# Kernel tuning notes

Measured on AMD Instinct MI355X. Metric: run time of the kernel, lower is better.

## Reference

```python
import jax, jax.numpy as jnp
import numpy as np

QLEN, BSZ, DM, NH, DH, FF = 1024, 4, 512, 8, 64, 2048
EPS = 1e-5


def layer_norm(x, g, b):
    mu = x.mean(-1, keepdims=True)
    var = ((x - mu) ** 2).mean(-1, keepdims=True)
    return (x - mu) / jnp.sqrt(var + EPS) * g + b


def rel_pos_emb(qlen, klen, d_model, bsz):
    # XLNet-style 'bi' relative positional encoding: positions klen .. -qlen+1
    freq = jnp.arange(0, d_model, 2, dtype=jnp.float32)
    inv_freq = 1.0 / (10000.0 ** (freq / d_model))
    pos_seq = jnp.arange(klen, -qlen, -1, dtype=jnp.float32)  # [klen+qlen]
    sinusoid = pos_seq[:, None] * inv_freq[None, :]           # [klen+qlen, d/2]
    pe = jnp.concatenate([jnp.sin(sinusoid), jnp.cos(sinusoid)], -1)
    return jnp.broadcast_to(pe[:, None, :], (pe.shape[0], bsz, d_model))


def rel_shift(x, klen):
    # x: [q, p, b, n] with p = klen + qlen
    q, p, b, n = x.shape
    x = x.reshape(p, q, b, n)[1:]
    x = x.reshape(q, p - 1, b, n)[:, :klen]
    return x


def setup_inputs() -> dict:
    key = jax.random.key(0)
    ks = jax.random.split(key, 20)
    s = 0.02
    inp = {
        'src': jax.random.normal(ks[0], (QLEN, BSZ, DM), jnp.float32),
        'q_w': jax.random.normal(ks[1], (DM, NH, DH), jnp.float32) * s,
        'k_w': jax.random.normal(ks[2], (DM, NH, DH), jnp.float32) * s,
        'v_w': jax.random.normal(ks[3], (DM, NH, DH), jnp.float32) * s,
        'r_w': jax.random.normal(ks[4], (DM, NH, DH), jnp.float32) * s,
        'o_w': jax.random.normal(ks[5], (DM, NH, DH), jnp.float32) * s,
        'r_w_bias': jax.random.normal(ks[6], (NH, DH), jnp.float32) * s,
        'r_r_bias': jax.random.normal(ks[7], (NH, DH), jnp.float32) * s,
        'w1': jax.random.normal(ks[8], (FF, DM), jnp.float32) * s,
        'b1': jnp.zeros((FF,), jnp.float32),
        'w2': jax.random.normal(ks[9], (DM, FF), jnp.float32) * s,
        'b2': jnp.zeros((DM,), jnp.float32),
        'g1': jnp.ones((DM,), jnp.float32), 'be1': jnp.zeros((DM,), jnp.float32),
        'g2': jnp.ones((DM,), jnp.float32), 'be2': jnp.zeros((DM,), jnp.float32),
        'gf': jnp.ones((DM,), jnp.float32), 'bf': jnp.zeros((DM,), jnp.float32),
        'src_mask': jnp.triu(jnp.ones((QLEN, QLEN), bool), k=1),
    }
    return inp


def reference(src, q_w, k_w, v_w, r_w, o_w, r_w_bias, r_r_bias,
              w1, b1, w2, b2, g1, be1, g2, be2, gf, bf, src_mask):
    qlen, bsz, dm = src.shape
    klen = qlen  # mems=None
    scale = 1.0 / (DH ** 0.5)
    pos_emb = rel_pos_emb(qlen, klen, dm, bsz)  # [klen+qlen, b, d]
    mask = src_mask.astype(src.dtype)

    # --- RelativeMultiheadAttention (single weight-shared encoder layer) ---
    cat = src  # no memory
    q_head = jnp.einsum('ibh,hnd->ibnd', src, q_w)
    k_head = jnp.einsum('ibh,hnd->ibnd', cat, k_w)
    v_head = jnp.einsum('ibh,hnd->ibnd', cat, v_w)
    k_pos = jnp.einsum('ibh,hnd->ibnd', pos_emb, r_w)

    ac = jnp.einsum('ibnd,jbnd->ijbn', q_head + r_w_bias, k_head)
    bd = jnp.einsum('ibnd,jbnd->ijbn', q_head + r_r_bias, k_pos)
    bd = rel_shift(bd, klen)

    score = (ac + bd) * scale - 1e30 * mask[:, :, None, None]
    prob = jax.nn.softmax(score, axis=1)
    attn_vec = jnp.einsum('ijbn,jbnd->ibnd', prob, v_head)
    attn_out = jnp.einsum('ibnd,hnd->ibh', attn_vec, o_w)

    x = layer_norm(src + attn_out, g1, be1)
    ffn = jax.nn.gelu(x @ w1.T + b1, approximate=False) @ w2.T + b2
    x = layer_norm(x + ffn, g2, be2)

    # final encoder norm
    out = layer_norm(x, gf, bf)
    return out
```

## Files before the change

### kernel.cpp

```cpp
#include <hip/hip_runtime.h>

#define QLEN 1024
#define BSZ  4
#define DM   512
#define NH   8
#define DH   64
#define FFD  2048

static constexpr float LN_EPS = 1e-5f;

typedef __attribute__((ext_vector_type(8))) short short8_t;
typedef __attribute__((ext_vector_type(4))) float f32x4;

__device__ __forceinline__ ushort f2b(float f) {
  uint u = __float_as_uint(f);
  return (ushort)((u + 0x7FFFu + ((u >> 16) & 1u)) >> 16);
}
__device__ __forceinline__ float b2f(ushort h) {
  return __uint_as_float(((uint)h) << 16);
}

__device__ __forceinline__ void cvt8_body(const float* in, ushort* out, int idx) {
  const float4 f0 = *reinterpret_cast<const float4*>(in + (size_t)idx * 8);
  const float4 f1 = *reinterpret_cast<const float4*>(in + (size_t)idx * 8 + 4);
  uint p0 = f2b(f0.x) | ((uint)f2b(f0.y) << 16);
  uint p1 = f2b(f0.z) | ((uint)f2b(f0.w) << 16);
  uint p2 = f2b(f1.x) | ((uint)f2b(f1.y) << 16);
  uint p3 = f2b(f1.z) | ((uint)f2b(f1.w) << 16);
  int4 st; st.x = (int)p0; st.y = (int)p1; st.z = (int)p2; st.w = (int)p3;
  *reinterpret_cast<int4*>(out + (size_t)idx * 8) = st;
}

__global__ __launch_bounds__(256) void prep_kernel(
    const float* __restrict__ src, const float* __restrict__ o_w,
    const float* __restrict__ w1, const float* __restrict__ w2,
    const float* __restrict__ qw, const float* __restrict__ kw,
    const float* __restrict__ vw, const float* __restrict__ rw,
    ushort* __restrict__ peb, ushort* __restrict__ srcb,
    ushort* __restrict__ owb, ushort* __restrict__ w1b,
    ushort* __restrict__ w2b, ushort* __restrict__ qkvw,
    ushort* __restrict__ rwT) {
  __shared__ float tile[32][33];
  const int bid = blockIdx.x, t = threadIdx.x;
  if (bid < 2048) {
    const int idx = bid * 256 + t;
    const int r = idx >> 9, f = idx & 511, f0 = f & 255;
    float invf = __expf(-(float)f0 * (9.210340371976184f / 256.0f));
    float arg  = (float)r * invf;
    peb[idx] = f2b((f < 256) ? __sinf(arg) : __cosf(arg));
  } else if (bid < 3072) {
    cvt8_body(src, srcb, (bid - 2048) * 256 + t);
  } else if (bid < 3200) {
    cvt8_body(o_w, owb, (bid - 3072) * 256 + t);
  } else if (bid < 3712) {
    cvt8_body(w1, w1b, (bid - 3200) * 256 + t);
  } else if (bid < 4224) {
    cvt8_body(w2, w2b, (bid - 3712) * 256 + t);
  } else {
    const int e = bid - 4224;
    const int z = e >> 8, rem = e & 255, bx = rem & 15, by = rem >> 4;
    const float* in = (z == 0) ? qw : (z == 1) ? kw : (z == 2) ? vw : rw;
    const int nd0 = bx * 32, h0 = by * 32;
    const int tx = t & 31, ty = t >> 5;
#pragma unroll
    for (int k = 0; k < 4; ++k)
      tile[ty + 8 * k][tx] = in[(size_t)(h0 + ty + 8 * k) * 512 + nd0 + tx];
    __syncthreads();
    ushort* out = (z < 3) ? (qkvw + (size_t)z * 512 * 512) : rwT;
#pragma unroll
    for (int k = 0; k < 4; ++k)
      out[(size_t)(nd0 + ty + 8 * k) * 512 + h0 + tx] = f2b(tile[tx][ty + 8 * k]);
  }
}

__device__ __forceinline__ void gemm128_body(
    const ushort* A, const ushort* B, ushort* C,
    int N, int K, int bm, int bn, int t,
    ushort* As, ushort* Bs) {
  const int w = t >> 6, l = t & 63;
  const int lc = l & 15, lq = l >> 4;
  const int wr = (w >> 1) * 64, wc = (w & 1) * 64;
  const int sr = t >> 2, sk = (t & 3) * 8;

  f32x4 acc[4][4];
#pragma unroll
  for (int i = 0; i < 4; ++i)
#pragma unroll
    for (int j = 0; j < 4; ++j) acc[i][j] = (f32x4){0.f, 0.f, 0.f, 0.f};

  int4 a0v = *reinterpret_cast<const int4*>(A + (size_t)(bm + sr) * K + sk);
  int4 a1v = *reinterpret_cast<const int4*>(A + (size_t)(bm + 64 + sr) * K + sk);
  int4 b0v = *reinterpret_cast<const int4*>(B + (size_t)(bn + sr) * K + sk);
  int4 b1v = *reinterpret_cast<const int4*>(B + (size_t)(bn + 64 + sr) * K + sk);

  for (int k0 = 0; k0 < K; k0 += 32) {
    *reinterpret_cast<int4*>(As + sr * 40 + sk) = a0v;
    *reinterpret_cast<int4*>(As + (64 + sr) * 40 + sk) = a1v;
    *reinterpret_cast<int4*>(Bs + sr * 40 + sk) = b0v;
    *reinterpret_cast<int4*>(Bs + (64 + sr) * 40 + sk) = b1v;
    __syncthreads();
    if (k0 + 32 < K) {
      a0v = *reinterpret_cast<const int4*>(A + (size_t)(bm + sr) * K + k0 + 32 + sk);
      a1v = *reinterpret_cast<const int4*>(A + (size_t)(bm + 64 + sr) * K + k0 + 32 + sk);
      b0v = *reinterpret_cast<const int4*>(B + (size_t)(bn + sr) * K + k0 + 32 + sk);
      b1v = *reinterpret_cast<const int4*>(B + (size_t)(bn + 64 + sr) * K + k0 + 32 + sk);
    }
    short8_t af[4], bf[4];
#pragma unroll
    for (int mf = 0; mf < 4; ++mf)
      af[mf] = *reinterpret_cast<const short8_t*>(As + (wr + mf * 16 + lc) * 40 + lq * 8);
#pragma unroll
    for (int nf = 0; nf < 4; ++nf)
      bf[nf] = *reinterpret_cast<const short8_t*>(Bs + (wc + nf * 16 + lc) * 40 + lq * 8);
#pragma unroll
    for (int mf = 0; mf < 4; ++mf)
#pragma unroll
      for (int nf = 0; nf < 4; ++nf)
        acc[mf][nf] = __builtin_amdgcn_mfma_f32_16x16x32_bf16(af[mf], bf[nf], acc[mf][nf], 0, 0, 0);
    __syncthreads();
  }

#pragma unroll
  for (int mf = 0; mf < 4; ++mf)
#pragma unroll
    for (int nf = 0; nf < 4; ++nf) {
      const int col = bn + wc + nf * 16 + lc;
#pragma unroll
      for (int reg = 0; reg < 4; ++reg) {
        const int row = bm + wr + mf * 16 + lq * 4 + reg;
        C[(size_t)row * N + col] = f2b(acc[mf][nf][reg]);
      }
    }
}

__global__ __launch_bounds__(256) void gemm128_dual(
    const ushort* __restrict__ srcb, const ushort* __restrict__ qkvw,
    const ushort* __restrict__ peb, const ushort* __restrict__ rwT,
    ushort* __restrict__ qkv, ushort* __restrict__ kprel) {
  __shared__ ushort As[128 * 40];
  __shared__ ushort Bs[128 * 40];
  const int bid = blockIdx.x, t = threadIdx.x;
  if (bid < 384) {
    const int bx = bid % 12, by = bid / 12;
    gemm128_body(srcb, qkvw, qkv, 1536, 512, by * 128, bx * 128, t, As, Bs);
  } else {
    const int e = bid - 384;
    const int bx = e & 3, by = e >> 2;
    gemm128_body(peb, rwT, kprel, 512, 512, by * 128, bx * 128, t, As, Bs);
  }
}

__global__ __launch_bounds__(256) void gemm128_gelu(
    const ushort* __restrict__ A, const ushort* __restrict__ B,
    const float* __restrict__ bias, ushort* __restrict__ Cout,
    int M, int N, int K) {
  __shared__ ushort As[128 * 40];
  __shared__ ushort Bs[128 * 40];
  const int t = threadIdx.x;
  const int w = t >> 6, l = t & 63;
  const int lc = l & 15, lq = l >> 4;
  const int bm = blockIdx.y * 128, bn = blockIdx.x * 128;
  const int wr = (w >> 1) * 64, wc = (w & 1) * 64;
  const int sr = t >> 2, sk = (t & 3) * 8;

  f32x4 acc[4][4];
#pragma unroll
  for (int i = 0; i < 4; ++i)
#pragma unroll
    for (int j = 0; j < 4; ++j) acc[i][j] = (f32x4){0.f, 0.f, 0.f, 0.f};

  int4 a0v = *reinterpret_cast<const int4*>(A + (size_t)(bm + sr) * K + sk);
  int4 a1v = *reinterpret_cast<const int4*>(A + (size_t)(bm + 64 + sr) * K + sk);
  int4 b0v = *reinterpret_cast<const int4*>(B + (size_t)(bn + sr) * K + sk);
  int4 b1v = *reinterpret_cast<const int4*>(B + (size_t)(bn + 64 + sr) * K + sk);

  for (int k0 = 0; k0 < K; k0 += 32) {
    *reinterpret_cast<int4*>(As + sr * 40 + sk) = a0v;
    *reinterpret_cast<int4*>(As + (64 + sr) * 40 + sk) = a1v;
    *reinterpret_cast<int4*>(Bs + sr * 40 + sk) = b0v;
    *reinterpret_cast<int4*>(Bs + (64 + sr) * 40 + sk) = b1v;
    __syncthreads();
    if (k0 + 32 < K) {
      a0v = *reinterpret_cast<const int4*>(A + (size_t)(bm + sr) * K + k0 + 32 + sk);
      a1v = *reinterpret_cast<const int4*>(A + (size_t)(bm + 64 + sr) * K + k0 + 32 + sk);
      b0v = *reinterpret_cast<const int4*>(B + (size_t)(bn + sr) * K + k0 + 32 + sk);
      b1v = *reinterpret_cast<const int4*>(B + (size_t)(bn + 64 + sr) * K + k0 + 32 + sk);
    }
    short8_t af[4], bf[4];
#pragma unroll
    for (int mf = 0; mf < 4; ++mf)
      af[mf] = *reinterpret_cast<const short8_t*>(As + (wr + mf * 16 + lc) * 40 + lq * 8);
#pragma unroll
    for (int nf = 0; nf < 4; ++nf)
      bf[nf] = *reinterpret_cast<const short8_t*>(Bs + (wc + nf * 16 + lc) * 40 + lq * 8);
#pragma unroll
    for (int mf = 0; mf < 4; ++mf)
#pragma unroll
      for (int nf = 0; nf < 4; ++nf)
        acc[mf][nf] = __builtin_amdgcn_mfma_f32_16x16x32_bf16(af[mf], bf[nf], acc[mf][nf], 0, 0, 0);
    __syncthreads();
  }

#pragma unroll
  for (int mf = 0; mf < 4; ++mf)
#pragma unroll
    for (int nf = 0; nf < 4; ++nf) {
      const int col = bn + wc + nf * 16 + lc;
#pragma unroll
      for (int reg = 0; reg < 4; ++reg) {
        const int row = bm + wr + mf * 16 + lq * 4 + reg;
        float v = acc[mf][nf][reg] + bias[col];
        v = 0.5f * v * (1.0f + erff(v * 0.70710678118654752f));
        Cout[(size_t)row * N + col] = f2b(v);
      }
    }
}

__global__ __launch_bounds__(256) void gemm_split(
    const ushort* __restrict__ A, const ushort* __restrict__ B,
    float* __restrict__ Cout, int M, int N, int K, int halfK) {
  __shared__ ushort As[64 * 40];
  __shared__ ushort Bs[128 * 40];
  const int t = threadIdx.x;
  const int w = t >> 6, l = t & 63;
  const int lc = l & 15, lq = l >> 4;
  const int bm = blockIdx.y * 64, bn = blockIdx.x * 128;
  const int wr = (w >> 1) * 32, wc = (w & 1) * 64;
  const int sr = t >> 2, sk = (t & 3) * 8;
  const int kbeg = blockIdx.z * halfK, kend = kbeg + halfK;
  float* C = Cout + (size_t)blockIdx.z * M * N;

  f32x4 acc[2][4];
#pragma unroll
  for (int i = 0; i < 2; ++i)
#pragma unroll
    for (int j = 0; j < 4; ++j) acc[i][j] = (f32x4){0.f, 0.f, 0.f, 0.f};

  int4 a_v = *reinterpret_cast<const int4*>(A + (size_t)(bm + sr) * K + kbeg + sk);
  int4 b0v = *reinterpret_cast<const int4*>(B + (size_t)(bn + sr) * K + kbeg + sk);
  int4 b1v = *reinterpret_cast<const int4*>(B + (size_t)(bn + 64 + sr) * K + kbeg + sk);

  for (int k0 = kbeg; k0 < kend; k0 += 32) {
    *reinterpret_cast<int4*>(As + sr * 40 + sk) = a_v;
    *reinterpret_cast<int4*>(Bs + sr * 40 + sk) = b0v;
    *reinterpret_cast<int4*>(Bs + (64 + sr) * 40 + sk) = b1v;
    __syncthreads();
    if (k0 + 32 < kend) {
      a_v = *reinterpret_cast<const int4*>(A + (size_t)(bm + sr) * K + k0 + 32 + sk);
      b0v = *reinterpret_cast<const int4*>(B + (size_t)(bn + sr) * K + k0 + 32 + sk);
      b1v = *reinterpret_cast<const int4*>(B + (size_t)(bn + 64 + sr) * K + k0 + 32 + sk);
    }
    short8_t af[2], bf[4];
#pragma unroll
    for (int mf = 0; mf < 2; ++mf)
      af[mf] = *reinterpret_cast<const short8_t*>(As + (wr + mf * 16 + lc) * 40 + lq * 8);
#pragma unroll
    for (int nf = 0; nf < 4; ++nf)
      bf[nf] = *reinterpret_cast<const short8_t*>(Bs + (wc + nf * 16 + lc) * 40 + lq * 8);
#pragma unroll
    for (int mf = 0; mf < 2; ++mf)
#pragma unroll
      for (int nf = 0; nf < 4; ++nf)
        acc[mf][nf] = __builtin_amdgcn_mfma_f32_16x16x32_bf16(af[mf], bf[nf], acc[mf][nf], 0, 0, 0);
    __syncthreads();
  }

#pragma unroll
  for (int mf = 0; mf < 2; ++mf)
#pragma unroll
    for (int nf = 0; nf < 4; ++nf) {
      const int col = bn + wc + nf * 16 + lc;
#pragma unroll
      for (int reg = 0; reg < 4; ++reg) {
        const int row = bm + wr + mf * 16 + lq * 4 + reg;
        C[(size_t)row * N + col] = acc[mf][nf][reg];
      }
    }
}

__global__ __launch_bounds__(256) void repack_kernel(
    const ushort* __restrict__ qkv, const float* __restrict__ rwb,
    const float* __restrict__ rrb, const ushort* __restrict__ kprel,
    ushort* __restrict__ qaF, ushort* __restrict__ qbF,
    ushort* __restrict__ kF, ushort* __restrict__ vF,
    ushort* __restrict__ kprelF) {
  __shared__ ushort st[32][72];
  const int bid = blockIdx.x, t = threadIdx.x;
  const int l = t & 63, lc = l & 15, lq = l >> 4;

  if (bid >= 3072) {
    if (t < 128) {
      const int e = bid - 3072;
      const int m = e % 66, n = e / 66;
      const int kc = t >> 6;
      const int rho = m * 16 - 31 + lc;
      short8_t v;
      if (rho >= 0 && rho < 1024)
        v = *reinterpret_cast<const short8_t*>(kprel + (size_t)rho * 512 + n * 64 + kc * 32 + lq * 8);
      else
#pragma unroll
        for (int e2 = 0; e2 < 8; ++e2) v[e2] = 0;
      const size_t o = ((size_t)((n * 66 + m) * 2 + kc)) * 512 + l * 8;
      *reinterpret_cast<short8_t*>(kprelF + o) = v;
    }
    return;
  }

  const int tile = bid & 31, head = (bid >> 5) & 31, role = bid >> 10;
  const int b = head >> 3, n = head & 7;
  const int s0 = tile * 32;
  const int sec = (role == 0) ? 0 : (role == 1) ? 512 : 1024;
  {
    const int s = t >> 3, d8 = (t & 7) * 8;
    int4 rd = *reinterpret_cast<const int4*>(
        qkv + (size_t)((s0 + s) * 4 + b) * 1536 + sec + n * 64 + d8);
    *reinterpret_cast<int4*>(&st[s][d8]) = rd;
  }
  __syncthreads();
  if (role == 0) {
    const int f = t >> 6, sub = f >> 1, kc = f & 1;
    const int row = sub * 16 + lc, k = kc * 32 + lq * 8;
    short8_t qv = *reinterpret_cast<const short8_t*>(&st[row][k]);
    const float4 w0 = *reinterpret_cast<const float4*>(rwb + n * 64 + k);
    const float4 w1 = *reinterpret_cast<const float4*>(rwb + n * 64 + k + 4);
    const float4 u0 = *reinterpret_cast<const float4*>(rrb + n * 64 + k);
    const float4 u1 = *reinterpret_cast<const float4*>(rrb + n * 64 + k + 4);
    const float wv[8] = {w0.x, w0.y, w0.z, w0.w, w1.x, w1.y, w1.z, w1.w};
    const float uv[8] = {u0.x, u0.y, u0.z, u0.w, u1.x, u1.y, u1.z, u1.w};
    short8_t a_, b_;
#pragma unroll
    for (int e = 0; e < 8; ++e) {
      float q = b2f((ushort)qv[e]);
      a_[e] = (short)f2b(q + wv[e]);
      b_[e] = (short)f2b(q + uv[e]);
    }
    const size_t o = ((size_t)((head * 64 + tile * 2 + sub) * 2 + kc)) * 512 + l * 8;
    *reinterpret_cast<short8_t*>(qaF + o) = a_;
    *reinterpret_cast<short8_t*>(qbF + o) = b_;
  } else if (role == 1) {
    const int f = t >> 6, sub = f >> 1, kc = f & 1;
    const int row = sub * 16 + lc, k = kc * 32 + lq * 8;
    short8_t kv = *reinterpret_cast<const short8_t*>(&st[row][k]);
    const size_t o = ((size_t)((head * 64 + tile * 2 + sub) * 2 + kc)) * 512 + l * 8;
    *reinterpret_cast<short8_t*>(kF + o) = kv;
  } else {
    const int nf = t >> 6;
    short8_t vv;
#pragma unroll
    for (int e = 0; e < 8; ++e) vv[e] = (short)st[lq * 8 + e][nf * 16 + lc];
    const size_t o = ((size_t)((head * 32 + tile) * 4 + nf)) * 512 + l * 8;
    *reinterpret_cast<short8_t*>(vF + o) = vv;
  }
}

__global__ __launch_bounds__(256, 4) void attn_mfma(
    const ushort* __restrict__ qaF, const ushort* __restrict__ qbF,
    const ushort* __restrict__ kF, const ushort* __restrict__ kpF,
    const ushort* __restrict__ vF, ushort* __restrict__ av) {
  __shared__ __align__(16) char smemU[5120];

  const int t = threadIdx.x, w = t >> 6, l = t & 63;
  const int lid = blockIdx.y * 32 + blockIdx.x;
  const int head = (lid & 7) * 4 + ((lid >> 3) & 3);
  const int pr   = lid >> 5;
  const int b = head >> 3, n = head & 7;
  const int lc = l & 15, lq = l >> 4;

  ushort* pw = reinterpret_cast<ushort*>(smemU) + w * (16 * 40);

  for (int ph = 0; ph < 2; ++ph) {
    const int it = ph ? 63 - pr : pr;
    const int i0 = it * 16;
    __syncthreads();

    short8_t qa[2], qb[2];
    {
      const size_t qo = ((size_t)(head * 64 + it) * 2) * 512 + l * 8;
      qa[0] = *reinterpret_cast<const short8_t*>(qaF + qo);
      qa[1] = *reinterpret_cast<const short8_t*>(qaF + qo + 512);
      qb[0] = *reinterpret_cast<const short8_t*>(qbF + qo);
      qb[1] = *reinterpret_cast<const short8_t*>(qbF + qo + 512);
    }

    float m_run[4], l_lane[4];
    f32x4 oacc[4];
#pragma unroll
    for (int reg = 0; reg < 4; ++reg) { m_run[reg] = -1e30f; l_lane[reg] = 0.f; }
#pragma unroll
    for (int nf = 0; nf < 4; ++nf) oacc[nf] = (f32x4){0.f, 0.f, 0.f, 0.f};

    const int nj = it / 2 + 1;

    for (int jt = w; jt < nj; jt += 4) {
      const int j0 = jt * 32;
      const int D = i0 - j0;

      f32x4 sacc[2];
#pragma unroll
      for (int nf = 0; nf < 2; ++nf) sacc[nf] = (f32x4){0.f, 0.f, 0.f, 0.f};
#pragma unroll
      for (int kc = 0; kc < 2; ++kc)
#pragma unroll
        for (int nf = 0; nf < 2; ++nf) {
          short8_t kf = *reinterpret_cast<const short8_t*>(
              kF + ((size_t)((head * 64 + (j0 >> 4) + nf) * 2 + kc)) * 512 + l * 8);
          sacc[nf] = __builtin_amdgcn_mfma_f32_16x16x32_bf16(qa[kc], kf, sacc[nf], 0, 0, 0);
        }

      f32x4 gacc[3];
#pragma unroll
      for (int nf = 0; nf < 3; ++nf) gacc[nf] = (f32x4){0.f, 0.f, 0.f, 0.f};
#pragma unroll
      for (int kc = 0; kc < 2; ++kc)
#pragma unroll
        for (int nf = 0; nf < 3; ++nf) {
          short8_t pf = *reinterpret_cast<const short8_t*>(
              kpF + ((size_t)((n * 66 + (D >> 4) + nf) * 2 + kc)) * 512 + l * 8);
          gacc[nf] = __builtin_amdgcn_mfma_f32_16x16x32_bf16(qb[kc], pf, gacc[nf], 0, 0, 0);
        }

      float s0v[4], s1v[4];
#pragma unroll
      for (int j = 0; j < 4; ++j) {
        const int r = lq * 4 + j;
        const int sl4 = ((((r + 15 - lc) & 15) | (lq << 4)) << 2);
        const float g0 = __int_as_float(__builtin_amdgcn_ds_bpermute(sl4, __float_as_int(gacc[0][j])));
        const float g1 = __int_as_float(__builtin_amdgcn_ds_bpermute(sl4, __float_as_int(gacc[1][j])));
        const float g2 = __int_as_float(__builtin_amdgcn_ds_bpermute(sl4, __float_as_int(gacc[2][j])));
        const bool sel = (r <= lc);
        const float Gu0 = sel ? g1 : g2;
        const float Gu1 = sel ? g0 : g1;
        float s0 = (sacc[0][j] + Gu0) * 0.125f;
        float s1 = (sacc[1][j] + Gu1) * 0.125f;
        if (D < 32) {
          if (lc > D + r) s0 = -1e30f;
          if (16 + lc > D + r) s1 = -1e30f;
        }
        s0v[j] = s0; s1v[j] = s1;
      }

      bool ok = true;
#pragma unroll
      for (int reg = 0; reg < 4; ++reg)
        ok &= (fmaxf(s0v[reg], s1v[reg]) <= m_run[reg] + 8.0f);
      if (__all(ok ? 1 : 0)) {
#pragma unroll
        for (int reg = 0; reg < 4; ++reg) {
          const int r = lq * 4 + reg;
          const float p0 = __expf(s0v[reg] - m_run[reg]);
          const float p1 = __expf(s1v[reg] - m_run[reg]);
          l_lane[reg] += p0 + p1;
          pw[r * 40 + lc] = f2b(p0);
          pw[r * 40 + 16 + lc] = f2b(p1);
        }
      } else {
#pragma unroll
        for (int reg = 0; reg < 4; ++reg) {
          const int r = lq * 4 + reg;
          float tm = fmaxf(s0v[reg], s1v[reg]);
          tm = fmaxf(tm, __shfl_xor(tm, 1));
          tm = fmaxf(tm, __shfl_xor(tm, 2));
          tm = fmaxf(tm, __shfl_xor(tm, 4));
          tm = fmaxf(tm, __shfl_xor(tm, 8));
          const float mn = fmaxf(m_run[reg], tm);
          const float corr = __expf(m_run[reg] - mn);
          const float p0 = __expf(s0v[reg] - mn), p1 = __expf(s1v[reg] - mn);
          l_lane[reg] = l_lane[reg] * corr + (p0 + p1);
          m_run[reg] = mn;
#pragma unroll
          for (int nf = 0; nf < 4; ++nf) oacc[nf][reg] *= corr;
          pw[r * 40 + lc] = f2b(p0);
          pw[r * 40 + 16 + lc] = f2b(p1);
        }
      }

      short8_t pa = *reinterpret_cast<const short8_t*>(pw + lc * 40 + lq * 8);
#pragma unroll
      for (int nf = 0; nf < 4; ++nf) {
        short8_t vf = *reinterpret_cast<const short8_t*>(
            vF + ((size_t)((head * 32 + jt) * 4 + nf)) * 512 + l * 8);
        oacc[nf] = __builtin_amdgcn_mfma_f32_16x16x32_bf16(pa, vf, oacc[nf], 0, 0, 0);
      }
    }

    float l_run[4];
#pragma unroll
    for (int reg = 0; reg < 4; ++reg) {
      float v = l_lane[reg];
      v += __shfl_xor(v, 1);
      v += __shfl_xor(v, 2);
      v += __shfl_xor(v, 4);
      v += __shfl_xor(v, 8);
      l_run[reg] = v;
    }

    __syncthreads();
    float* obuf = reinterpret_cast<float*>(smemU);
    float* mlb  = reinterpret_cast<float*>(smemU + 4352);

    if (lc == 0) {
#pragma unroll
      for (int reg = 0; reg < 4; ++reg) {
        const int r = lq * 4 + reg;
        mlb[(w * 16 + r) * 2 + 0] = m_run[reg];
        mlb[(w * 16 + r) * 2 + 1] = l_run[reg];
      }
    }
    for (int i = t; i < 16 * 68; i += 256) obuf[i] = 0.f;
    __syncthreads();

    float scl[4];
#pragma unroll
    for (int reg = 0; reg < 4; ++reg) {
      const int r = lq * 4 + reg;
      const float m0 = mlb[r * 2], m1 = mlb[(16 + r) * 2],
                  m2 = mlb[(32 + r) * 2], m3 = mlb[(48 + r) * 2];
      const float ms = fmaxf(fmaxf(m0, m1), fmaxf(m2, m3));
      scl[reg] = __expf(mlb[(w * 16 + r) * 2] - ms);
    }
#pragma unroll
    for (int ww = 0; ww < 4; ++ww) {
      if (w == ww) {
#pragma unroll
        for (int nf = 0; nf < 4; ++nf)
#pragma unroll
          for (int reg = 0; reg < 4; ++reg) {
            const int r = lq * 4 + reg;
            obuf[r * 68 + nf * 16 + lc] += scl[reg] * oacc[nf][reg];
          }
      }
      __syncthreads();
    }

    {
      const int r = t >> 4, d0 = (t & 15) * 4;
      const float m0 = mlb[r * 2], m1 = mlb[(16 + r) * 2],
                  m2 = mlb[(32 + r) * 2], m3 = mlb[(48 + r) * 2];
      const float ms = fmaxf(fmaxf(m0, m1), fmaxf(m2, m3));
      const float ls = mlb[r * 2 + 1] * __expf(m0 - ms) + mlb[(16 + r) * 2 + 1] * __expf(m1 - ms) +
                       mlb[(32 + r) * 2 + 1] * __expf(m2 - ms) + mlb[(48 + r) * 2 + 1] * __expf(m3 - ms);
      const float inv = 1.f / ls;
      uint pk0 = (uint)f2b(obuf[r * 68 + d0] * inv) | ((uint)f2b(obuf[r * 68 + d0 + 1] * inv) << 16);
      uint pk1 = (uint)f2b(obuf[r * 68 + d0 + 2] * inv) | ((uint)f2b(obuf[r * 68 + d0 + 3] * inv) << 16);
      int2 st2; st2.x = (int)pk0; st2.y = (int)pk1;
      const int tok = (i0 + r) * 4 + b;
      *reinterpret_cast<int2*>(av + (size_t)tok * 512 + n * 64 + d0) = st2;
    }
  }
}

__device__ __forceinline__ float blk_sum(float v, volatile float* sb) {
  v += __shfl_xor(v, 1);  v += __shfl_xor(v, 2);  v += __shfl_xor(v, 4);
  v += __shfl_xor(v, 8);  v += __shfl_xor(v, 16); v += __shfl_xor(v, 32);
  const int t = threadIdx.x;
  if ((t & 63) == 0) sb[t >> 6] = v;
  __syncthreads();
  v = sb[0] + sb[1] + sb[2] + sb[3];
  __syncthreads();
  return v;
}

__global__ __launch_bounds__(256) void ln_res_kernel(
    const float* __restrict__ aoa, const float* __restrict__ aob,
    const float* __restrict__ res,
    const float* __restrict__ g, const float* __restrict__ be,
    float* __restrict__ out, ushort* __restrict__ outb) {
  __shared__ float sb[4];
  const int row = blockIdx.x, t = threadIdx.x;
  const size_t base = (size_t)row * DM;
  const float x0 = aoa[base + t] + aob[base + t] + res[base + t];
  const float x1 = aoa[base + t + 256] + aob[base + t + 256] + res[base + t + 256];
  const float mu = blk_sum(x0 + x1, sb) * (1.f / DM);
  const float d0 = x0 - mu, d1 = x1 - mu;
  const float var = blk_sum(d0 * d0 + d1 * d1, sb) * (1.f / DM);
  const float inv = rsqrtf(var + LN_EPS);
  const float z0 = d0 * inv * g[t] + be[t];
  const float z1 = d1 * inv * g[t + 256] + be[t + 256];
  out[base + t] = z0;
  out[base + t + 256] = z1;
  outb[base + t] = f2b(z0);
  outb[base + t + 256] = f2b(z1);
}

__global__ __launch_bounds__(256) void ln_final_kernel(
    const float* __restrict__ ya, const float* __restrict__ yb,
    const float* __restrict__ b2, const float* __restrict__ xres,
    const float* __restrict__ g2, const float* __restrict__ be2,
    const float* __restrict__ gf, const float* __restrict__ bf,
    float* __restrict__ out) {
  __shared__ float sb[4];
  const int row = blockIdx.x, t = threadIdx.x;
  const size_t base = (size_t)row * DM;
  const float x0 = ya[base + t] + yb[base + t] + b2[t] + xres[base + t];
  const float x1 = ya[base + t + 256] + yb[base + t + 256] + b2[t + 256] + xres[base + t + 256];
  const float mu = blk_sum(x0 + x1, sb) * (1.f / DM);
  const float d0 = x0 - mu, d1 = x1 - mu;
  const float var = blk_sum(d0 * d0 + d1 * d1, sb) * (1.f / DM);
  const float inv = rsqrtf(var + LN_EPS);
  const float z0 = d0 * inv * g2[t] + be2[t];
  const float z1 = d1 * inv * g2[t + 256] + be2[t + 256];
  const float mu2 = blk_sum(z0 + z1, sb) * (1.f / DM);
  const float e0 = z0 - mu2, e1 = z1 - mu2;
  const float var2 = blk_sum(e0 * e0 + e1 * e1, sb) * (1.f / DM);
  const float inv2 = rsqrtf(var2 + LN_EPS);
  out[base + t]       = e0 * inv2 * gf[t] + bf[t];
  out[base + t + 256] = e1 * inv2 * gf[t + 256] + bf[t + 256];
}

extern "C" void kernel_launch(void* const* d_in, const int* in_sizes, int n_in,
                              void* d_out, int out_size, void* d_ws, size_t ws_size,
                              hipStream_t stream) {
  const float* src = (const float*)d_in[0];
  const float* q_w = (const float*)d_in[1];
  const float* k_w = (const float*)d_in[2];
  const float* v_w = (const float*)d_in[3];
  const float* r_w = (const float*)d_in[4];
  const float* o_w = (const float*)d_in[5];
  const float* rwb = (const float*)d_in[6];
  const float* rrb = (const float*)d_in[7];
  const float* w1  = (const float*)d_in[8];
  const float* b1  = (const float*)d_in[9];
  const float* w2  = (const float*)d_in[10];
  const float* b2  = (const float*)d_in[11];
  const float* g1  = (const float*)d_in[12];
  const float* be1 = (const float*)d_in[13];
  const float* g2  = (const float*)d_in[14];
  const float* be2 = (const float*)d_in[15];
  const float* gf  = (const float*)d_in[16];
  const float* bf  = (const float*)d_in[17];

  char* ws = (char*)d_ws;
  const size_t KB = 1024, MB = 1024 * 1024;
  ushort* srcb   = (ushort*)(ws);
  ushort* qkvw   = (ushort*)(ws + 4 * MB);
  ushort* rwT    = (ushort*)(ws + 5 * MB + 512 * KB);
  ushort* owb    = (ushort*)(ws + 6 * MB);
  ushort* w1b    = (ushort*)(ws + 6 * MB + 512 * KB);
  ushort* w2b    = (ushort*)(ws + 8 * MB + 512 * KB);
  ushort* peb    = (ushort*)(ws + 10 * MB + 512 * KB);
  ushort* qkv    = (ushort*)(ws + 11 * MB + 512 * KB);
  ushort* kprel  = (ushort*)(ws + 23 * MB + 512 * KB);
  ushort* qaF    = (ushort*)(ws + 24 * MB + 512 * KB);
  ushort* qbF    = (ushort*)(ws + 28 * MB + 512 * KB);
  ushort* kF     = (ushort*)(ws + 32 * MB + 512 * KB);
  ushort* vF     = (ushort*)(ws + 36 * MB + 512 * KB);
  ushort* kprelF = (ushort*)(ws + 40 * MB + 512 * KB);
  ushort* av     = (ushort*)(ws + 42 * MB);
  float*  aoP    = (float*) (ws + 24 * MB + 512 * KB);
  float*  x1     = (float*) (ws + 46 * MB);
  ushort* x1b    = (ushort*)(ws + 42 * MB);
  ushort* h      = (ushort*)(ws + 11 * MB + 512 * KB);
  float*  y2P    = (float*) (ws + 27 * MB + 512 * KB);
  float*  outp   = (float*)d_out;

  prep_kernel<<<dim3(5248), 256, 0, stream>>>(src, o_w, w1, w2, q_w, k_w, v_w, r_w,
                                              peb, srcb, owb, w1b, w2b, qkvw, rwT);

  gemm128_dual<<<dim3(416), 256, 0, stream>>>(srcb, qkvw, peb, rwT, qkv, kprel);

  repack_kernel<<<dim3(3600), 256, 0, stream>>>(qkv, rwb, rrb, kprel, qaF, qbF, kF, vF, kprelF);

  attn_mfma<<<dim3(32, 32), 256, 0, stream>>>(qaF, qbF, kF, kprelF, vF, av);

  gemm_split<<<dim3(4, 64, 2), 256, 0, stream>>>(av, owb, aoP, 4096, 512, 512, 256);
  ln_res_kernel<<<dim3(4096), 256, 0, stream>>>(aoP, aoP + 2097152, src, g1, be1, x1, x1b);

  gemm128_gelu<<<dim3(16, 32), 256, 0, stream>>>(x1b, w1b, b1, h, 4096, 2048, 512);
  gemm_split<<<dim3(4, 64, 2), 256, 0, stream>>>(h, w2b, y2P, 4096, 512, 2048, 1024);

  ln_final_kernel<<<dim3(4096), 256, 0, stream>>>(y2P, y2P + 2097152, b2, x1, g2, be2, gf, bf, outp);
}
```

Baseline: 134.3 us.

## Prefetch next K/pos tiles into registers and parallelize cross-wave output merge

In the causal attention kernel, each wave now loads the K and positional-key fragments for its next j-tile while it runs softmax on the current one, and loads V at the top of the iteration, so global load latency overlaps with compute. The epilogue no longer has waves accumulate into one shared buffer in turn with four barriers. Each wave writes its scaled partial output to its own LDS slab, and the final pass sums the four slabs. This raises register pressure and LDS use (about 17.5 KB per block), which may lower occupancy under the 4-blocks-per-SM launch bound.

Result: slower. 220.8 us (+64.4%).

```diff
diff --git a/kernel.cpp b/kernel.cpp
--- a/kernel.cpp
+++ b/kernel.cpp
@@ -357,7 +357,7 @@
     const ushort* __restrict__ qaF, const ushort* __restrict__ qbF,
     const ushort* __restrict__ kF, const ushort* __restrict__ kpF,
     const ushort* __restrict__ vF, ushort* __restrict__ av) {
-  __shared__ __align__(16) char smemU[5120];
+  __shared__ __align__(16) char smemU[17920];
 
   const int t = threadIdx.x, w = t >> 6, l = t & 63;
   const int lid = blockIdx.y * 32 + blockIdx.x;
@@ -367,6 +367,27 @@
   const int lc = l & 15, lq = l >> 4;
 
   ushort* pw = reinterpret_cast<ushort*>(smemU) + w * (16 * 40);
+
+#define LOADK(dst, jt_)                                                        \
+  {                                                                            \
+    const int jb16 = ((jt_) * 32) >> 4;                                        \
+    _Pragma("unroll")                                                          \
+    for (int kc = 0; kc < 2; ++kc)                                             \
+      _Pragma("unroll")                                                        \
+      for (int nf = 0; nf < 2; ++nf)                                           \
+        dst[kc][nf] = *reinterpret_cast<const short8_t*>(                      \
+            kF + ((size_t)((head * 64 + jb16 + nf) * 2 + kc)) * 512 + l * 8);  \
+  }
+#define LOADP(dst, jt_)                                                        \
+  {                                                                            \
+    const int Dm = (i0 - (jt_) * 32) >> 4;                                     \
+    _Pragma("unroll")                                                          \
+    for (int kc = 0; kc < 2; ++kc)                                             \
+      _Pragma("unroll")                                                        \
+      for (int nf = 0; nf < 3; ++nf)                                           \
+        dst[kc][nf] = *reinterpret_cast<const short8_t*>(                      \
+            kpF + ((size_t)((n * 66 + Dm + nf) * 2 + kc)) * 512 + l * 8);      \
+  }
 
   for (int ph = 0; ph < 2; ++ph) {
     const int it = ph ? 63 - pr : pr;
@@ -391,9 +412,19 @@
 
     const int nj = it / 2 + 1;
 
+    short8_t kfA[2][2], pfA[2][3];
+    if (w < nj) { LOADK(kfA, w); LOADP(pfA, w); }
+
     for (int jt = w; jt < nj; jt += 4) {
       const int j0 = jt * 32;
       const int D = i0 - j0;
+      const int jn = jt + 4;
+
+      short8_t vfv[4];
+#pragma unroll
+      for (int nf = 0; nf < 4; ++nf)
+        vfv[nf] = *reinterpret_cast<const short8_t*>(
+            vF + ((size_t)((head * 32 + jt) * 4 + nf)) * 512 + l * 8);
 
       f32x4 sacc[2];
 #pragma unroll
@@ -401,11 +432,8 @@
 #pragma unroll
       for (int kc = 0; kc < 2; ++kc)
 #pragma unroll
-        for (int nf = 0; nf < 2; ++nf) {
-          short8_t kf = *reinterpret_cast<const short8_t*>(
-              kF + ((size_t)((head * 64 + (j0 >> 4) + nf) * 2 + kc)) * 512 + l * 8);
-          sacc[nf] = __builtin_amdgcn_mfma_f32_16x16x32_bf16(qa[kc], kf, sacc[nf], 0, 0, 0);
-        }
+        for (int nf = 0; nf < 2; ++nf)
+          sacc[nf] = __builtin_amdgcn_mfma_f32_16x16x32_bf16(qa[kc], kfA[kc][nf], sacc[nf], 0, 0, 0);
 
       f32x4 gacc[3];
 #pragma unroll
@@ -413,11 +441,11 @@
 #pragma unroll
       for (int kc = 0; kc < 2; ++kc)
 #pragma unroll
-        for (int nf = 0; nf < 3; ++nf) {
-          short8_t pf = *reinterpret_cast<const short8_t*>(
-              kpF + ((size_t)((n * 66 + (D >> 4) + nf) * 2 + kc)) * 512 + l * 8);
-          gacc[nf] = __builtin_amdgcn_mfma_f32_16x16x32_bf16(qb[kc], pf, gacc[nf], 0, 0, 0);
-        }
+        for (int nf = 0; nf < 3; ++nf)
+          gacc[nf] = __builtin_amdgcn_mfma_f32_16x16x32_bf16(qb[kc], pfA[kc][nf], gacc[nf], 0, 0, 0);
+
+      short8_t kfB[2][2], pfB[2][3];
+      if (jn < nj) { LOADK(kfB, jn); LOADP(pfB, jn); }
 
       float s0v[4], s1v[4];
 #pragma unroll
@@ -476,10 +504,15 @@
 
       short8_t pa = *reinterpret_cast<const short8_t*>(pw + lc * 40 + lq * 8);
 #pragma unroll
-      for (int nf = 0; nf < 4; ++nf) {
-        short8_t vf = *reinterpret_cast<const short8_t*>(
-            vF + ((size_t)((head * 32 + jt) * 4 + nf)) * 512 + l * 8);
-        oacc[nf] = __builtin_amdgcn_mfma_f32_16x16x32_bf16(pa, vf, oacc[nf], 0, 0, 0);
+      for (int nf = 0; nf < 4; ++nf)
+        oacc[nf] = __builtin_amdgcn_mfma_f32_16x16x32_bf16(pa, vfv[nf], oacc[nf], 0, 0, 0);
+
+#pragma unroll
+      for (int kc = 0; kc < 2; ++kc) {
+#pragma unroll
+        for (int nf = 0; nf < 2; ++nf) kfA[kc][nf] = kfB[kc][nf];
+#pragma unroll
+        for (int nf = 0; nf < 3; ++nf) pfA[kc][nf] = pfB[kc][nf];
       }
     }
 
@@ -496,7 +529,8 @@
 
     __syncthreads();
     float* obuf = reinterpret_cast<float*>(smemU);
-    float* mlb  = reinterpret_cast<float*>(smemU + 4352);
+    float* mlb  = reinterpret_cast<float*>(smemU + 17408);
+    float* ow   = obuf + w * (16 * 68);
 
     if (lc == 0) {
 #pragma unroll
@@ -506,7 +540,6 @@
         mlb[(w * 16 + r) * 2 + 1] = l_run[reg];
       }
     }
-    for (int i = t; i < 16 * 68; i += 256) obuf[i] = 0.f;
     __syncthreads();
 
     float scl[4];
@@ -519,18 +552,13 @@
       scl[reg] = __expf(mlb[(w * 16 + r) * 2] - ms);
     }
 #pragma unroll
-    for (int ww = 0; ww < 4; ++ww) {
-      if (w == ww) {
-#pragma unroll
-        for (int nf = 0; nf < 4; ++nf)
-#pragma unroll
-          for (int reg = 0; reg < 4; ++reg) {
-            const int r = lq * 4 + reg;
-            obuf[r * 68 + nf * 16 + lc] += scl[reg] * oacc[nf][reg];
-          }
-      }
-      __syncthreads();
-    }
+    for (int nf = 0; nf < 4; ++nf)
+#pragma unroll
+      for (int reg = 0; reg < 4; ++reg) {
+        const int r = lq * 4 + reg;
+        ow[r * 68 + nf * 16 + lc] = scl[reg] * oacc[nf][reg];
+      }
+    __syncthreads();
 
     {
       const int r = t >> 4, d0 = (t & 15) * 4;
@@ -540,13 +568,22 @@
       const float ls = mlb[r * 2 + 1] * __expf(m0 - ms) + mlb[(16 + r) * 2 + 1] * __expf(m1 - ms) +
                        mlb[(32 + r) * 2 + 1] * __expf(m2 - ms) + mlb[(48 + r) * 2 + 1] * __expf(m3 - ms);
       const float inv = 1.f / ls;
-      uint pk0 = (uint)f2b(obuf[r * 68 + d0] * inv) | ((uint)f2b(obuf[r * 68 + d0 + 1] * inv) << 16);
-      uint pk1 = (uint)f2b(obuf[r * 68 + d0 + 2] * inv) | ((uint)f2b(obuf[r * 68 + d0 + 3] * inv) << 16);
+      float o4[4];
+#pragma unroll
+      for (int e = 0; e < 4; ++e) {
+        const int c = d0 + e;
+        o4[e] = (obuf[r * 68 + c] + obuf[16 * 68 + r * 68 + c] +
+                 obuf[2 * 16 * 68 + r * 68 + c] + obuf[3 * 16 * 68 + r * 68 + c]) * inv;
+      }
+      uint pk0 = (uint)f2b(o4[0]) | ((uint)f2b(o4[1]) << 16);
+      uint pk1 = (uint)f2b(o4[2]) | ((uint)f2b(o4[3]) << 16);
       int2 st2; st2.x = (int)pk0; st2.y = (int)pk1;
       const int tok = (i0 + r) * 4 + b;
       *reinterpret_cast<int2*>(av + (size_t)tok * 512 + n * 64 + d0) = st2;
     }
   }
+#undef LOADK
+#undef LOADP
 }
 
 __device__ __forceinline__ float blk_sum(float v, volatile float* sb) {
```
